# Optimization experiments

Measured on AMD Instinct MI355X. Metric: run time of the kernel, lower is better.

## Reference

```python
import jax, jax.numpy as jnp
import numpy as np

B, T, D, H, L = 128, 512, 64, 512, 256  # batch, max_seq_len, input_dim, hidden_dim, latent_dim


def setup_inputs() -> dict:
    key = jax.random.key(0)
    ks = jax.random.split(key, 12)
    x = jax.random.normal(ks[0], (B, T, D), dtype=jnp.float32)
    lengths = jax.random.randint(ks[1], (B,), 1, T + 1)
    lengths = lengths.at[0].set(T)  # ensure max(lengths) == T for static shapes
    s = 0.05
    p = lambda k, shp: jax.random.normal(k, shp, dtype=jnp.float32) * s
    return {
        "x": x, "lengths": lengths,
        # encoder LSTM (PyTorch gate order i,f,g,o); b = b_ih + b_hh fused
        "W_ih_e": p(ks[2], (4 * H, D)), "W_hh_e": p(ks[3], (4 * H, H)), "b_e": p(ks[4], (4 * H,)),
        "W_lat": p(ks[5], (L, H)), "b_lat": p(ks[6], (L,)),
        # decoder LSTM
        "W_ih_d": p(ks[7], (4 * H, L)), "W_hh_d": p(ks[8], (4 * H, H)), "b_d": p(ks[9], (4 * H,)),
        "W_out": p(ks[10], (D, H)), "b_out": p(ks[11], (D,)),
    }


def _lstm_cell(gates, c):
    # gates: [B, 4H] pre-activations in PyTorch order (input, forget, cell, output)
    i = jax.nn.sigmoid(gates[:, :H])
    f = jax.nn.sigmoid(gates[:, H:2 * H])
    g = jnp.tanh(gates[:, 2 * H:3 * H])
    o = jax.nn.sigmoid(gates[:, 3 * H:])
    c_new = f * c + i * g
    h_new = o * jnp.tanh(c_new)
    return h_new, c_new


def reference(x, lengths, W_ih_e, W_hh_e, b_e, W_lat, b_lat, W_ih_d, W_hh_d, b_d, W_out, b_out):
    mask = jnp.arange(T)[:, None] < lengths[None, :]  # [T, B] valid-step mask
    # Precompute input contributions for all timesteps: [T, B, 4H]
    gx = jnp.einsum('btd,gd->tbg', x, W_ih_e) + b_e
    h0 = jnp.zeros((B, H), x.dtype)
    c0 = jnp.zeros((B, H), x.dtype)

    # Encoder: packed semantics == freeze (h, c) once t >= length, so final h
    # equals the hidden state at each sequence's last valid step.
    def enc_step(carry, inp):
        h, c = carry
        g, m = inp
        h_new, c_new = _lstm_cell(g + h @ W_hh_e.T, c)
        m = m[:, None]
        return (jnp.where(m, h_new, h), jnp.where(m, c_new, c)), None

    (h_n, _), _ = jax.lax.scan(enc_step, (h0, c0), (gx, mask))
    z = h_n @ W_lat.T + b_lat  # [B, L]

    # Decoder input is z repeated at every valid step -> constant per-step input term.
    zx = z @ W_ih_d.T + b_d  # [B, 4H]

    def dec_step(carry, m):
        h, c = carry
        h_new, c_new = _lstm_cell(zx + h @ W_hh_d.T, c)
        m = m[:, None]
        h2 = jnp.where(m, h_new, h)
        c2 = jnp.where(m, c_new, c)
        y = jnp.where(m, h2, jnp.zeros_like(h2))  # pad_packed_sequence zero-pads outputs
        return (h2, c2), y

    _, ys = jax.lax.scan(dec_step, (h0, c0), mask)  # [T, B, H]
    # Padded positions: ys == 0, so output there is exactly b_out (matches torch).
    out = jnp.einsum('tbh,dh->btd', ys, W_out) + b_out  # [B, T, D]
    return out
```

## Files before the change

kernel.cpp:

```cpp
#include <hip/hip_runtime.h>
#include <cstdint>

constexpr int NB = 128;
constexpr int NT = 512;
constexpr int ND = 64;
constexpr int NH = 512;
constexpr int NL = 256;

typedef _Float16 half8 __attribute__((ext_vector_type(8)));
typedef float F4 __attribute__((ext_vector_type(4)));
typedef uint32_t u32;
typedef unsigned long long u64;
typedef uint32_t u32x4 __attribute__((ext_vector_type(4)));

constexpr size_t OFF_WFE = 0;
constexpr size_t OFF_WFD = (2u << 20);
constexpr size_t OFF_WFX = (4u << 20);
constexpr size_t OFF_WFO = (4u << 20) + (256u << 10);
constexpr size_t OFF_XF  = (4u << 20) + (320u << 10);
constexpr size_t OFF_RE  = (12u << 20) + (320u << 10);
constexpr size_t OFF_RD  = (13u << 20) + (320u << 10);
constexpr size_t OFF_Z   = (14u << 20) + (320u << 10);
constexpr size_t OFF_ZX  = (14u << 20) + (448u << 10);

__device__ inline float sigm(float x) {
  float e = __expf(-fabsf(x));
  float p = 1.f / (1.f + e);
  return x >= 0.f ? p : 1.f - p;
}
__device__ inline float tanh_(float x) {
  float e = __expf(-2.f * fabsf(x));
  float t = (1.f - e) / (1.f + e);
  return x >= 0.f ? t : -t;
}
__device__ inline half8 cvt8(F4 a, F4 b) {
  half8 h;
  h[0] = (_Float16)a[0]; h[1] = (_Float16)a[1]; h[2] = (_Float16)a[2]; h[3] = (_Float16)a[3];
  h[4] = (_Float16)b[0]; h[5] = (_Float16)b[1]; h[6] = (_Float16)b[2]; h[7] = (_Float16)b[3];
  return h;
}

__global__ __launch_bounds__(256) void setup_kernel(
    const float* __restrict__ x, const float* __restrict__ W_hh_e,
    const float* __restrict__ W_ih_e, const float* __restrict__ W_hh_d,
    const float* __restrict__ W_out,
    half8* __restrict__ WfE, half8* __restrict__ WfX, half8* __restrict__ WfD,
    half8* __restrict__ WfO, half8* __restrict__ Xf) {
  int c = blockIdx.x * 256 + threadIdx.x;
  if (c < 131072) {
    int hc = c >> 12, g = (c >> 10) & 3, tt = (c >> 6) & 15, l = c & 63;
    int col = g * 512 + hc * 16 + (l & 15);
    int k8 = 4 * tt + (l >> 4);
    const F4* s = (const F4*)(W_hh_e + (size_t)col * 512 + k8 * 8);
    WfE[c] = cvt8(s[0], s[1]);
  } else if (c < 147456) {
    int id = c - 131072;
    int hc = id >> 9, g = (id >> 7) & 3, tx = (id >> 6) & 1, l = id & 63;
    int col = g * 512 + hc * 16 + (l & 15);
    int k8 = 4 * tx + (l >> 4);
    const F4* s = (const F4*)(W_ih_e + (size_t)col * 64 + k8 * 8);
    WfX[id] = cvt8(s[0], s[1]);
  } else if (c < 278528) {
    int id = c - 147456;
    int hc = id >> 12, g = (id >> 10) & 3, tt = (id >> 6) & 15, l = id & 63;
    int col = g * 512 + hc * 16 + (l & 15);
    int k8 = 4 * tt + (l >> 4);
    const F4* s = (const F4*)(W_hh_d + (size_t)col * 512 + k8 * 8);
    WfD[id] = cvt8(s[0], s[1]);
  } else if (c < 282624) {
    int id = c - 278528;
    int dt = id >> 10, k = (id >> 6) & 15, l = id & 63;
    int d = dt * 16 + (l & 15);
    int k8 = k * 4 + (l >> 4);
    const F4* s = (const F4*)(W_out + (size_t)d * 512 + k8 * 8);
    WfO[id] = cvt8(s[0], s[1]);
  } else {
    int id = c - 282624;
    int t = id >> 10, bi = (id >> 7) & 7, k8 = (id >> 4) & 7, row = id & 15;
    const F4* s = (const F4*)(x + ((size_t)(bi * 16 + row) * NT + t) * ND + k8 * 8);
    Xf[id] = cvt8(s[0], s[1]);
  }
}

#define PIN4(v) asm volatile("" : "+v"(v.x), "+v"(v.y), "+v"(v.z), "+v"(v.w))

#define STAGE_H(RINGT, TAG)                                                      \
  {                                                                              \
    const u64* bp = (RINGT) + ((size_t)((TAG) & 3) * 16 + srow) * 256;           \
    u64 v[16];                                                                   \
    for (;;) {                                                                   \
      _Pragma("unroll")                                                          \
      for (int j = 0; j < 16; j++)                                               \
        v[j] = __hip_atomic_load(bp + (scb + 16 * (j >> 2)) * 4 + (j & 3),       \
                                 __ATOMIC_RELAXED, __HIP_MEMORY_SCOPE_AGENT);    \
      bool ok = true;                                                            \
      _Pragma("unroll")                                                          \
      for (int j = 0; j < 16; j++) ok &= ((u32)(v[j] >> 32) == (u32)(TAG));      \
      if (ok) break;                                                             \
      __builtin_amdgcn_s_sleep(1);                                               \
    }                                                                            \
    _Pragma("unroll")                                                            \
    for (int j = 0; j < 4; j++) {                                                \
      int cc = scb + 16 * j;                                                     \
      u32x4 u = {(u32)v[4 * j], (u32)v[4 * j + 1], (u32)v[4 * j + 2],            \
                 (u32)v[4 * j + 3]};                                             \
      Hlds[srow * 64 + (cc ^ (srow & 7))] = u;                                   \
    }                                                                            \
  }

__global__ __launch_bounds__(256, 1) void enc_persist(
    const uint4* __restrict__ Wf, const uint4* __restrict__ Wfx,
    const uint4* __restrict__ Xf, u64* __restrict__ Ring,
    const float* __restrict__ b_e, const int* __restrict__ lengths) {
  const int tid = threadIdx.x;
  const int l = tid & 63, g = tid >> 6;
  const int bi = (int)blockIdx.x & 7, w = (int)blockIdx.x >> 3;
  __shared__ u32x4 Hlds[1024];
  __shared__ float gl[4][16][17];
  __shared__ unsigned short hst[16][16];

  uint4 wb[16];
#pragma unroll
  for (int k = 0; k < 16; k++) {
    wb[k] = Wf[(size_t)w * 4096 + (g * 16 + k) * 64 + l];
    PIN4(wb[k]);
  }
  uint4 wx0 = Wfx[(size_t)w * 512 + (g * 2 + 0) * 64 + l];
  uint4 wx1 = Wfx[(size_t)w * 512 + (g * 2 + 1) * 64 + l];
  PIN4(wx0); PIN4(wx1);

  const int row = tid >> 4, col = tid & 15;
  const int b = bi * 16 + row;
  const int len = lengths[b];
  const float be0 = b_e[w * 16 + col], be1 = b_e[512 + w * 16 + col];
  const float be2 = b_e[1024 + w * 16 + col], be3 = b_e[1536 + w * 16 + col];
  float cst = 0.f, hreg = 0.f;
  const int srow = tid >> 4, scb = tid & 15;
  u64* ringT = Ring + (size_t)bi * (4 * 16 * 256);
  const int ar = l & 15, swz = ar & 7, r0 = (l >> 4) * 4;

  for (int t = 0; t < NT; t++) {
    if (t > 0) {
      STAGE_H(ringT, t);
      __syncthreads();
    }
    F4 acc0 = {0.f, 0.f, 0.f, 0.f}, acc1 = {0.f, 0.f, 0.f, 0.f};
    if (t > 0) {
#pragma unroll
      for (int k = 0; k < 16; k += 2) {
        u32x4 a0 = Hlds[ar * 64 + (((l >> 4) + 4 * k) ^ swz)];
        u32x4 a1 = Hlds[ar * 64 + (((l >> 4) + 4 * (k + 1)) ^ swz)];
        acc0 = __builtin_amdgcn_mfma_f32_16x16x32_f16(
            __builtin_bit_cast(half8, a0), __builtin_bit_cast(half8, wb[k]), acc0, 0, 0, 0);
        acc1 = __builtin_amdgcn_mfma_f32_16x16x32_f16(
            __builtin_bit_cast(half8, a1), __builtin_bit_cast(half8, wb[k + 1]), acc1, 0, 0, 0);
      }
    }
    uint4 xa0 = Xf[((size_t)t * 8 + bi) * 128 + l];
    uint4 xa1 = Xf[((size_t)t * 8 + bi) * 128 + 64 + l];
    acc0 = __builtin_amdgcn_mfma_f32_16x16x32_f16(
        __builtin_bit_cast(half8, xa0), __builtin_bit_cast(half8, wx0), acc0, 0, 0, 0);
    acc1 = __builtin_amdgcn_mfma_f32_16x16x32_f16(
        __builtin_bit_cast(half8, xa1), __builtin_bit_cast(half8, wx1), acc1, 0, 0, 0);
    F4 acc = acc0 + acc1;
#pragma unroll
    for (int r = 0; r < 4; r++) gl[g][r0 + r][ar] = acc[r];
    __syncthreads();

    float hv;
    if (t < len) {
      float gi = gl[0][row][col] + be0;
      float gf = gl[1][row][col] + be1;
      float gg = gl[2][row][col] + be2;
      float go = gl[3][row][col] + be3;
      float i = sigm(gi), f = sigm(gf), gz = tanh_(gg), o = sigm(go);
      cst = f * cst + i * gz;
      hv = o * tanh_(cst);
    } else {
      hv = hreg;
    }
    hreg = hv;
    hst[row][col] = __builtin_bit_cast(unsigned short, (_Float16)hv);
    __syncthreads();

    if (tid < 128) {
      int pr = tid >> 3, pk = tid & 7;
      u32 lo = (u32)hst[pr][2 * pk] | ((u32)hst[pr][2 * pk + 1] << 16);
      u64 vv = ((u64)(u32)(t + 1) << 32) | lo;
      __hip_atomic_store(ringT + ((size_t)((t + 1) & 3) * 16 + pr) * 256 + w * 8 + pk,
                         vv, __ATOMIC_RELAXED, __HIP_MEMORY_SCOPE_AGENT);
    }
  }
}

__global__ __launch_bounds__(256) void z_kernel(const u64* __restrict__ RingE,
                                                const float* __restrict__ W_lat,
                                                const float* __restrict__ b_lat,
                                                float* __restrict__ Z) {
  int b = blockIdx.x, lc = threadIdx.x;
  int bi = b >> 4, row = b & 15;
  const u64* hp = RingE + ((size_t)(bi * 4 + (NT & 3)) * 16 + row) * 256;
  float acc = 0.f;
  for (int j = 0; j < 256; j++) {
    u32 lo = (u32)hp[j];
    float h0 = (float)__builtin_bit_cast(_Float16, (unsigned short)(lo & 0xFFFF));
    float h1 = (float)__builtin_bit_cast(_Float16, (unsigned short)(lo >> 16));
    acc += h0 * W_lat[(size_t)lc * 512 + 2 * j] + h1 * W_lat[(size_t)lc * 512 + 2 * j + 1];
  }
  Z[(size_t)b * 256 + lc] = acc + b_lat[lc];
}

__global__ __launch_bounds__(256) void zx_kernel(const float* __restrict__ Z,
                                                 const float* __restrict__ W_ihd,
                                                 const float* __restrict__ b_d,
                                                 float* __restrict__ ZX) {
  int o = blockIdx.x * 256 + threadIdx.x;
  int b = o >> 11, gc = o & 2047;
  const F4* zp = (const F4*)(Z + (size_t)b * 256);
  const F4* wp = (const F4*)(W_ihd + (size_t)gc * 256);
  float acc = 0.f;
  for (int k4 = 0; k4 < 64; k4++) {
    F4 z = zp[k4], wv = wp[k4];
    acc += z[0] * wv[0] + z[1] * wv[1] + z[2] * wv[2] + z[3] * wv[3];
  }
  ZX[o] = acc + b_d[gc];
}

__global__ __launch_bounds__(256, 1) void dec_persist(
    const uint4* __restrict__ Wf, const uint4* __restrict__ WfO,
    u64* __restrict__ Ring, const float* __restrict__ ZX,
    const float* __restrict__ b_out, float* __restrict__ out,
    const int* __restrict__ lengths) {
  const int tid = threadIdx.x;
  const int l = tid & 63, g = tid >> 6;
  const int bi = (int)blockIdx.x & 7, w = (int)blockIdx.x >> 3;
  __shared__ u32x4 Hlds[1024];
  __shared__ float gl[4][16][17];
  __shared__ unsigned short hst[16][16];

  uint4 wb[16], wo[16];
#pragma unroll
  for (int k = 0; k < 16; k++) {
    wb[k] = Wf[(size_t)w * 4096 + (g * 16 + k) * 64 + l];
    wo[k] = WfO[(size_t)g * 1024 + k * 64 + l];
    PIN4(wb[k]); PIN4(wo[k]);
  }

  const int row = tid >> 4, col = tid & 15;
  const int b = bi * 16 + row;
  const int len = lengths[b];
  const int lenA = lengths[bi * 16 + (l & 15)];
  const float bo = b_out[g * 16 + (l & 15)];
  const float zr0 = ZX[(size_t)b * 2048 + w * 16 + col];
  const float zr1 = ZX[(size_t)b * 2048 + 512 + w * 16 + col];
  const float zr2 = ZX[(size_t)b * 2048 + 1024 + w * 16 + col];
  const float zr3 = ZX[(size_t)b * 2048 + 1536 + w * 16 + col];
  float cst = 0.f, hreg = 0.f;
  const int srow = tid >> 4, scb = tid & 15;
  u64* ringT = Ring + (size_t)bi * (4 * 16 * 256);
  const int ar = l & 15, swz = ar & 7, r0 = (l >> 4) * 4;

  for (int t = 0; t <= NT; t++) {
    if (t == NT && w != 31) break;
    if (t > 0) {
      STAGE_H(ringT, t);
      __syncthreads();
    }
    if (t < NT) {
      F4 acc0 = {0.f, 0.f, 0.f, 0.f}, acc1 = {0.f, 0.f, 0.f, 0.f};
      if (t > 0) {
#pragma unroll
        for (int k = 0; k < 16; k += 2) {
          u32x4 a0 = Hlds[ar * 64 + (((l >> 4) + 4 * k) ^ swz)];
          u32x4 a1 = Hlds[ar * 64 + (((l >> 4) + 4 * (k + 1)) ^ swz)];
          acc0 = __builtin_amdgcn_mfma_f32_16x16x32_f16(
              __builtin_bit_cast(half8, a0), __builtin_bit_cast(half8, wb[k]), acc0, 0, 0, 0);
          acc1 = __builtin_amdgcn_mfma_f32_16x16x32_f16(
              __builtin_bit_cast(half8, a1), __builtin_bit_cast(half8, wb[k + 1]), acc1, 0, 0, 0);
        }
      }
      F4 acc = acc0 + acc1;
#pragma unroll
      for (int r = 0; r < 4; r++) gl[g][r0 + r][ar] = acc[r];
      __syncthreads();

      float hv;
      if (t < len) {
        float gi = gl[0][row][col] + zr0;
        float gf = gl[1][row][col] + zr1;
        float gg = gl[2][row][col] + zr2;
        float go = gl[3][row][col] + zr3;
        float i = sigm(gi), f = sigm(gf), gz = tanh_(gg), o = sigm(go);
        cst = f * cst + i * gz;
        hv = o * tanh_(cst);
      } else {
        hv = hreg;
      }
      hreg = hv;
      hst[row][col] = __builtin_bit_cast(unsigned short, (_Float16)hv);
      __syncthreads();

      if (tid < 128) {
        int pr = tid >> 3, pk = tid & 7;
        u32 lo = (u32)hst[pr][2 * pk] | ((u32)hst[pr][2 * pk + 1] << 16);
        u64 vv = ((u64)(u32)(t + 1) << 32) | lo;
        __hip_atomic_store(ringT + ((size_t)((t + 1) & 3) * 16 + pr) * 256 + w * 8 + pk,
                           vv, __ATOMIC_RELAXED, __HIP_MEMORY_SCOPE_AGENT);
      }
    }
    if (t > 0 && w == ((t - 1) & 31)) {
      bool ma = (t - 1) < lenA;
      F4 oa0 = {0.f, 0.f, 0.f, 0.f}, oa1 = {0.f, 0.f, 0.f, 0.f};
      u32x4 zer = {0u, 0u, 0u, 0u};
#pragma unroll
      for (int k = 0; k < 16; k += 2) {
        u32x4 a0 = ma ? Hlds[ar * 64 + (((l >> 4) + 4 * k) ^ swz)] : zer;
        u32x4 a1 = ma ? Hlds[ar * 64 + (((l >> 4) + 4 * (k + 1)) ^ swz)] : zer;
        oa0 = __builtin_amdgcn_mfma_f32_16x16x32_f16(
            __builtin_bit_cast(half8, a0), __builtin_bit_cast(half8, wo[k]), oa0, 0, 0, 0);
        oa1 = __builtin_amdgcn_mfma_f32_16x16x32_f16(
            __builtin_bit_cast(half8, a1), __builtin_bit_cast(half8, wo[k + 1]), oa1, 0, 0, 0);
      }
      F4 oa = oa0 + oa1;
#pragma unroll
      for (int r = 0; r < 4; r++)
        out[((size_t)(bi * 16 + r0 + r) * NT + (t - 1)) * 64 + g * 16 + (l & 15)] = oa[r] + bo;
    }
  }
}

extern "C" void kernel_launch(void* const* d_in, const int* in_sizes, int n_in,
                              void* d_out, int out_size, void* d_ws, size_t ws_size,
                              hipStream_t stream) {
  const float* x      = (const float*)d_in[0];
  const int* lengths  = (const int*)d_in[1];
  const float* W_ih_e = (const float*)d_in[2];
  const float* W_hh_e = (const float*)d_in[3];
  const float* b_e    = (const float*)d_in[4];
  const float* W_lat  = (const float*)d_in[5];
  const float* b_lat  = (const float*)d_in[6];
  const float* W_ih_d = (const float*)d_in[7];
  const float* W_hh_d = (const float*)d_in[8];
  const float* b_d    = (const float*)d_in[9];
  const float* W_out  = (const float*)d_in[10];
  const float* b_out  = (const float*)d_in[11];
  float* out = (float*)d_out;
  char* ws = (char*)d_ws;

  half8* WfE = (half8*)(ws + OFF_WFE);
  half8* WfD = (half8*)(ws + OFF_WFD);
  half8* WfX = (half8*)(ws + OFF_WFX);
  half8* WfO = (half8*)(ws + OFF_WFO);
  half8* Xf  = (half8*)(ws + OFF_XF);
  u64* RingE = (u64*)(ws + OFF_RE);
  u64* RingD = (u64*)(ws + OFF_RD);
  float* Z  = (float*)(ws + OFF_Z);
  float* ZX = (float*)(ws + OFF_ZX);

  hipMemsetAsync(RingE, 0, 2u << 20, stream);
  setup_kernel<<<3152, 256, 0, stream>>>(x, W_hh_e, W_ih_e, W_hh_d, W_out,
                                         WfE, WfX, WfD, WfO, Xf);

  enc_persist<<<256, 256, 0, stream>>>((const uint4*)WfE, (const uint4*)WfX,
                                       (const uint4*)Xf, RingE, b_e, lengths);
  z_kernel<<<128, 256, 0, stream>>>(RingE, W_lat, b_lat, Z);
  zx_kernel<<<1024, 256, 0, stream>>>(Z, W_ih_d, b_d, ZX);
  dec_persist<<<256, 256, 0, stream>>>((const uint4*)WfD, (const uint4*)WfO,
                                       RingD, ZX, b_out, out, lengths);
}
```

Measured before the change: 3.946 ms.

## Split inter-block hidden-state exchange into separate data and per-wave tag arrays

Replaces the tagged 64-bit ring entries (data plus step tag in every word) with a packed fp16 data buffer and a small per-wave tag array. Consumers poll only 128 tags with a wave-wide vote, then read the data once. Producers pack h via lane shuffles, removing the LDS staging buffer and one block barrier per step. The x-projection load is also hoisted ahead of the wait, and the decoder's output projection is restructured. The cost is an extra release-style wait (vmcnt) before each tag store, and correctness depends on ordering between relaxed stores.

New measurement: 6.788 ms. +72.0%, slower.

```diff
diff --git a/kernel.cpp b/kernel.cpp
--- a/kernel.cpp
+++ b/kernel.cpp
@@ -18,10 +18,12 @@
 constexpr size_t OFF_WFX = (4u << 20);
 constexpr size_t OFF_WFO = (4u << 20) + (256u << 10);
 constexpr size_t OFF_XF  = (4u << 20) + (320u << 10);
-constexpr size_t OFF_RE  = (12u << 20) + (320u << 10);
-constexpr size_t OFF_RD  = (13u << 20) + (320u << 10);
-constexpr size_t OFF_Z   = (14u << 20) + (320u << 10);
-constexpr size_t OFF_ZX  = (14u << 20) + (448u << 10);
+constexpr size_t OFF_DE  = (12u << 20) + (320u << 10);
+constexpr size_t OFF_DD  = OFF_DE + (512u << 10);
+constexpr size_t OFF_TE  = OFF_DD + (512u << 10);
+constexpr size_t OFF_TD  = OFF_TE + (64u << 10);
+constexpr size_t OFF_Z   = OFF_TD + (64u << 10);
+constexpr size_t OFF_ZX  = OFF_Z + (128u << 10);
 
 __device__ inline float sigm(float x) {
   float e = __expf(-fabsf(x));
@@ -39,6 +41,10 @@
   h[4] = (_Float16)b[0]; h[5] = (_Float16)b[1]; h[6] = (_Float16)b[2]; h[7] = (_Float16)b[3];
   return h;
 }
+
+#define PIN4(v) asm volatile("" : "+v"(v.x), "+v"(v.y), "+v"(v.z), "+v"(v.w))
+#define MFMA(A, B, C) __builtin_amdgcn_mfma_f32_16x16x32_f16( \
+    __builtin_bit_cast(half8, A), __builtin_bit_cast(half8, B), C, 0, 0, 0)
 
 __global__ __launch_bounds__(256) void setup_kernel(
     const float* __restrict__ x, const float* __restrict__ W_hh_e,
@@ -82,89 +88,99 @@
   }
 }
 
-#define PIN4(v) asm volatile("" : "+v"(v.x), "+v"(v.y), "+v"(v.z), "+v"(v.w))
-
-#define STAGE_H(RINGT, TAG)                                                      \
-  {                                                                              \
-    const u64* bp = (RINGT) + ((size_t)((TAG) & 3) * 16 + srow) * 256;           \
-    u64 v[16];                                                                   \
-    for (;;) {                                                                   \
-      _Pragma("unroll")                                                          \
-      for (int j = 0; j < 16; j++)                                               \
-        v[j] = __hip_atomic_load(bp + (scb + 16 * (j >> 2)) * 4 + (j & 3),       \
-                                 __ATOMIC_RELAXED, __HIP_MEMORY_SCOPE_AGENT);    \
-      bool ok = true;                                                            \
-      _Pragma("unroll")                                                          \
-      for (int j = 0; j < 16; j++) ok &= ((u32)(v[j] >> 32) == (u32)(TAG));      \
-      if (ok) break;                                                             \
-      __builtin_amdgcn_s_sleep(1);                                               \
-    }                                                                            \
-    _Pragma("unroll")                                                            \
-    for (int j = 0; j < 4; j++) {                                                \
-      int cc = scb + 16 * j;                                                     \
-      u32x4 u = {(u32)v[4 * j], (u32)v[4 * j + 1], (u32)v[4 * j + 2],            \
-                 (u32)v[4 * j + 3]};                                             \
-      Hlds[srow * 64 + (cc ^ (srow & 7))] = u;                                   \
-    }                                                                            \
+#define POLL_TAGS(TT, T)                                                        \
+  for (;;) {                                                                    \
+    u32 ta = __hip_atomic_load((TT) + l, __ATOMIC_RELAXED,                      \
+                               __HIP_MEMORY_SCOPE_AGENT);                       \
+    u32 tb = __hip_atomic_load((TT) + 64 + l, __ATOMIC_RELAXED,                 \
+                               __HIP_MEMORY_SCOPE_AGENT);                       \
+    if (__all(ta >= (u32)(T) && tb >= (u32)(T))) break;                         \
+  }
+
+#define STAGE_DATA(DT, T)                                                       \
+  {                                                                             \
+    const u64* dp = (DT) + (size_t)((T) & 3) * 2048 + srow * 128 + scb * 8;     \
+    u64 v[8];                                                                   \
+    _Pragma("unroll")                                                           \
+    for (int j = 0; j < 8; j++)                                                 \
+      v[j] = __hip_atomic_load(dp + j, __ATOMIC_RELAXED,                        \
+                               __HIP_MEMORY_SCOPE_AGENT);                       \
+    _Pragma("unroll")                                                           \
+    for (int j = 0; j < 8; j++) {                                               \
+      int cc = scb * 4 + (j >> 1);                                              \
+      *(u64*)&lds32[srow * 256 + ((cc ^ (srow & 7)) << 2) + (j & 1) * 2] = v[j];\
+    }                                                                           \
+  }
+
+#define PUBLISH(DT, TT, HV, T)                                                  \
+  {                                                                             \
+    u32 self = (u32)__builtin_bit_cast(unsigned short, (_Float16)(HV));         \
+    u32 part = (u32)__shfl_xor((int)self, 1);                                   \
+    u32 p32 = (l & 1) ? ((self << 16) | part) : ((part << 16) | self);          \
+    u32 q = (u32)__shfl_xor((int)p32, 2);                                       \
+    u64 p64 = (l & 2) ? (((u64)p32 << 32) | q) : (((u64)q << 32) | p32);        \
+    if ((l & 3) == 0)                                                           \
+      __hip_atomic_store((DT) + (size_t)(((T) + 1) & 3) * 2048 +                \
+                             (size_t)row * 128 + w * 4 + ((l >> 2) & 3),        \
+                         p64, __ATOMIC_RELAXED, __HIP_MEMORY_SCOPE_AGENT);      \
+    asm volatile("s_waitcnt vmcnt(0)" ::: "memory");                            \
+    if (l == 0)                                                                 \
+      __hip_atomic_store((TT) + w * 4 + g, (u32)((T) + 1), __ATOMIC_RELAXED,    \
+                         __HIP_MEMORY_SCOPE_AGENT);                             \
   }
 
 __global__ __launch_bounds__(256, 1) void enc_persist(
     const uint4* __restrict__ Wf, const uint4* __restrict__ Wfx,
-    const uint4* __restrict__ Xf, u64* __restrict__ Ring,
+    const uint4* __restrict__ Xf, u64* __restrict__ Data, u32* __restrict__ Tag,
     const float* __restrict__ b_e, const int* __restrict__ lengths) {
   const int tid = threadIdx.x;
   const int l = tid & 63, g = tid >> 6;
   const int bi = (int)blockIdx.x & 7, w = (int)blockIdx.x >> 3;
-  __shared__ u32x4 Hlds[1024];
+  __shared__ u32 lds32[4096];
   __shared__ float gl[4][16][17];
-  __shared__ unsigned short hst[16][16];
 
   uint4 wb[16];
 #pragma unroll
-  for (int k = 0; k < 16; k++) {
-    wb[k] = Wf[(size_t)w * 4096 + (g * 16 + k) * 64 + l];
-    PIN4(wb[k]);
-  }
+  for (int k = 0; k < 16; k++) wb[k] = Wf[(size_t)w * 4096 + (g * 16 + k) * 64 + l];
   uint4 wx0 = Wfx[(size_t)w * 512 + (g * 2 + 0) * 64 + l];
   uint4 wx1 = Wfx[(size_t)w * 512 + (g * 2 + 1) * 64 + l];
-  PIN4(wx0); PIN4(wx1);
 
   const int row = tid >> 4, col = tid & 15;
-  const int b = bi * 16 + row;
-  const int len = lengths[b];
+  const int len = lengths[bi * 16 + row];
   const float be0 = b_e[w * 16 + col], be1 = b_e[512 + w * 16 + col];
   const float be2 = b_e[1024 + w * 16 + col], be3 = b_e[1536 + w * 16 + col];
   float cst = 0.f, hreg = 0.f;
   const int srow = tid >> 4, scb = tid & 15;
-  u64* ringT = Ring + (size_t)bi * (4 * 16 * 256);
-  const int ar = l & 15, swz = ar & 7, r0 = (l >> 4) * 4;
+  u64* DT = Data + (size_t)bi * 8192;
+  u32* TT = Tag + bi * 128;
+  const int ar = l & 15, swz = ar & 7, r0v = (l >> 4) * 4;
 
   for (int t = 0; t < NT; t++) {
-    if (t > 0) {
-      STAGE_H(ringT, t);
-      __syncthreads();
-    }
-    F4 acc0 = {0.f, 0.f, 0.f, 0.f}, acc1 = {0.f, 0.f, 0.f, 0.f};
-    if (t > 0) {
-#pragma unroll
-      for (int k = 0; k < 16; k += 2) {
-        u32x4 a0 = Hlds[ar * 64 + (((l >> 4) + 4 * k) ^ swz)];
-        u32x4 a1 = Hlds[ar * 64 + (((l >> 4) + 4 * (k + 1)) ^ swz)];
-        acc0 = __builtin_amdgcn_mfma_f32_16x16x32_f16(
-            __builtin_bit_cast(half8, a0), __builtin_bit_cast(half8, wb[k]), acc0, 0, 0, 0);
-        acc1 = __builtin_amdgcn_mfma_f32_16x16x32_f16(
-            __builtin_bit_cast(half8, a1), __builtin_bit_cast(half8, wb[k + 1]), acc1, 0, 0, 0);
-      }
-    }
+#pragma unroll
+    for (int k = 0; k < 16; k++) PIN4(wb[k]);
+    PIN4(wx0); PIN4(wx1);
     uint4 xa0 = Xf[((size_t)t * 8 + bi) * 128 + l];
     uint4 xa1 = Xf[((size_t)t * 8 + bi) * 128 + 64 + l];
-    acc0 = __builtin_amdgcn_mfma_f32_16x16x32_f16(
-        __builtin_bit_cast(half8, xa0), __builtin_bit_cast(half8, wx0), acc0, 0, 0, 0);
-    acc1 = __builtin_amdgcn_mfma_f32_16x16x32_f16(
-        __builtin_bit_cast(half8, xa1), __builtin_bit_cast(half8, wx1), acc1, 0, 0, 0);
+    if (t > 0) {
+      POLL_TAGS(TT, t);
+      STAGE_DATA(DT, t);
+      __syncthreads();
+    }
+    F4 acc0 = {0.f, 0.f, 0.f, 0.f}, acc1 = {0.f, 0.f, 0.f, 0.f};
+    acc0 = MFMA(xa0, wx0, acc0);
+    acc1 = MFMA(xa1, wx1, acc1);
+    if (t > 0) {
+#pragma unroll
+      for (int k = 0; k < 16; k += 2) {
+        u32x4 a0 = *(u32x4*)&lds32[ar * 256 + (((4 * k + (l >> 4)) ^ swz) << 2)];
+        u32x4 a1 = *(u32x4*)&lds32[ar * 256 + (((4 * (k + 1) + (l >> 4)) ^ swz) << 2)];
+        acc0 = MFMA(a0, wb[k], acc0);
+        acc1 = MFMA(a1, wb[k + 1], acc1);
+      }
+    }
     F4 acc = acc0 + acc1;
 #pragma unroll
-    for (int r = 0; r < 4; r++) gl[g][r0 + r][ar] = acc[r];
+    for (int r = 0; r < 4; r++) gl[g][r0v + r][ar] = acc[r];
     __syncthreads();
 
     float hv;
@@ -180,29 +196,20 @@
       hv = hreg;
     }
     hreg = hv;
-    hst[row][col] = __builtin_bit_cast(unsigned short, (_Float16)hv);
-    __syncthreads();
-
-    if (tid < 128) {
-      int pr = tid >> 3, pk = tid & 7;
-      u32 lo = (u32)hst[pr][2 * pk] | ((u32)hst[pr][2 * pk + 1] << 16);
-      u64 vv = ((u64)(u32)(t + 1) << 32) | lo;
-      __hip_atomic_store(ringT + ((size_t)((t + 1) & 3) * 16 + pr) * 256 + w * 8 + pk,
-                         vv, __ATOMIC_RELAXED, __HIP_MEMORY_SCOPE_AGENT);
-    }
-  }
-}
-
-__global__ __launch_bounds__(256) void z_kernel(const u64* __restrict__ RingE,
+    PUBLISH(DT, TT, hv, t);
+  }
+}
+
+__global__ __launch_bounds__(256) void z_kernel(const u32* __restrict__ DataE,
                                                 const float* __restrict__ W_lat,
                                                 const float* __restrict__ b_lat,
                                                 float* __restrict__ Z) {
   int b = blockIdx.x, lc = threadIdx.x;
   int bi = b >> 4, row = b & 15;
-  const u64* hp = RingE + ((size_t)(bi * 4 + (NT & 3)) * 16 + row) * 256;
+  const u32* hp = DataE + (size_t)bi * 16384 + (size_t)row * 256;
   float acc = 0.f;
   for (int j = 0; j < 256; j++) {
-    u32 lo = (u32)hp[j];
+    u32 lo = hp[j];
     float h0 = (float)__builtin_bit_cast(_Float16, (unsigned short)(lo & 0xFFFF));
     float h1 = (float)__builtin_bit_cast(_Float16, (unsigned short)(lo >> 16));
     acc += h0 * W_lat[(size_t)lc * 512 + 2 * j] + h1 * W_lat[(size_t)lc * 512 + 2 * j + 1];
@@ -226,24 +233,40 @@
   ZX[o] = acc + b_d[gc];
 }
 
+#define OUT_PROJ(TCUR)                                                           \
+  {                                                                              \
+    bool ma = ((TCUR) < lenA);                                                   \
+    F4 oa0 = {0.f, 0.f, 0.f, 0.f}, oa1 = {0.f, 0.f, 0.f, 0.f};                   \
+    u32x4 zer = {0u, 0u, 0u, 0u};                                                \
+    _Pragma("unroll")                                                            \
+    for (int k = 0; k < 16; k += 2) {                                            \
+      u32x4 a0 = ma ? *(u32x4*)&lds32[ar * 256 + (((4 * k + (l >> 4)) ^ swz) << 2)] : zer; \
+      u32x4 a1 = ma ? *(u32x4*)&lds32[ar * 256 + (((4 * (k + 1) + (l >> 4)) ^ swz) << 2)] : zer; \
+      oa0 = MFMA(a0, wo[k], oa0);                                                \
+      oa1 = MFMA(a1, wo[k + 1], oa1);                                            \
+    }                                                                            \
+    F4 oa = oa0 + oa1;                                                           \
+    _Pragma("unroll")                                                            \
+    for (int r = 0; r < 4; r++)                                                  \
+      out[((size_t)(bi * 16 + r0v + r) * NT + (TCUR)) * 64 + g * 16 + (l & 15)] = oa[r] + bo; \
+  }
+
 __global__ __launch_bounds__(256, 1) void dec_persist(
     const uint4* __restrict__ Wf, const uint4* __restrict__ WfO,
-    u64* __restrict__ Ring, const float* __restrict__ ZX,
+    u64* __restrict__ Data, u32* __restrict__ Tag, const float* __restrict__ ZX,
     const float* __restrict__ b_out, float* __restrict__ out,
     const int* __restrict__ lengths) {
   const int tid = threadIdx.x;
   const int l = tid & 63, g = tid >> 6;
   const int bi = (int)blockIdx.x & 7, w = (int)blockIdx.x >> 3;
-  __shared__ u32x4 Hlds[1024];
+  __shared__ u32 lds32[4096];
   __shared__ float gl[4][16][17];
-  __shared__ unsigned short hst[16][16];
 
   uint4 wb[16], wo[16];
 #pragma unroll
   for (int k = 0; k < 16; k++) {
     wb[k] = Wf[(size_t)w * 4096 + (g * 16 + k) * 64 + l];
     wo[k] = WfO[(size_t)g * 1024 + k * 64 + l];
-    PIN4(wb[k]); PIN4(wo[k]);
   }
 
   const int row = tid >> 4, col = tid & 15;
@@ -257,75 +280,57 @@
   const float zr3 = ZX[(size_t)b * 2048 + 1536 + w * 16 + col];
   float cst = 0.f, hreg = 0.f;
   const int srow = tid >> 4, scb = tid & 15;
-  u64* ringT = Ring + (size_t)bi * (4 * 16 * 256);
-  const int ar = l & 15, swz = ar & 7, r0 = (l >> 4) * 4;
-
-  for (int t = 0; t <= NT; t++) {
-    if (t == NT && w != 31) break;
+  u64* DT = Data + (size_t)bi * 8192;
+  u32* TT = Tag + bi * 128;
+  const int ar = l & 15, swz = ar & 7, r0v = (l >> 4) * 4;
+
+  for (int t = 0; t < NT; t++) {
+#pragma unroll
+    for (int k = 0; k < 16; k++) { PIN4(wb[k]); PIN4(wo[k]); }
     if (t > 0) {
-      STAGE_H(ringT, t);
+      POLL_TAGS(TT, t);
+      STAGE_DATA(DT, t);
       __syncthreads();
     }
-    if (t < NT) {
-      F4 acc0 = {0.f, 0.f, 0.f, 0.f}, acc1 = {0.f, 0.f, 0.f, 0.f};
-      if (t > 0) {
-#pragma unroll
-        for (int k = 0; k < 16; k += 2) {
-          u32x4 a0 = Hlds[ar * 64 + (((l >> 4) + 4 * k) ^ swz)];
-          u32x4 a1 = Hlds[ar * 64 + (((l >> 4) + 4 * (k + 1)) ^ swz)];
-          acc0 = __builtin_amdgcn_mfma_f32_16x16x32_f16(
-              __builtin_bit_cast(half8, a0), __builtin_bit_cast(half8, wb[k]), acc0, 0, 0, 0);
-          acc1 = __builtin_amdgcn_mfma_f32_16x16x32_f16(
-              __builtin_bit_cast(half8, a1), __builtin_bit_cast(half8, wb[k + 1]), acc1, 0, 0, 0);
-        }
+    F4 acc0 = {0.f, 0.f, 0.f, 0.f}, acc1 = {0.f, 0.f, 0.f, 0.f};
+    if (t > 0) {
+#pragma unroll
+      for (int k = 0; k < 16; k += 2) {
+        u32x4 a0 = *(u32x4*)&lds32[ar * 256 + (((4 * k + (l >> 4)) ^ swz) << 2)];
+        u32x4 a1 = *(u32x4*)&lds32[ar * 256 + (((4 * (k + 1) + (l >> 4)) ^ swz) << 2)];
+        acc0 = MFMA(a0, wb[k], acc0);
+        acc1 = MFMA(a1, wb[k + 1], acc1);
       }
-      F4 acc = acc0 + acc1;
-#pragma unroll
-      for (int r = 0; r < 4; r++) gl[g][r0 + r][ar] = acc[r];
-      __syncthreads();
-
-      float hv;
-      if (t < len) {
-        float gi = gl[0][row][col] + zr0;
-        float gf = gl[1][row][col] + zr1;
-        float gg = gl[2][row][col] + zr2;
-        float go = gl[3][row][col] + zr3;
-        float i = sigm(gi), f = sigm(gf), gz = tanh_(gg), o = sigm(go);
-        cst = f * cst + i * gz;
-        hv = o * tanh_(cst);
-      } else {
-        hv = hreg;
-      }
-      hreg = hv;
-      hst[row][col] = __builtin_bit_cast(unsigned short, (_Float16)hv);
-      __syncthreads();
-
-      if (tid < 128) {
-        int pr = tid >> 3, pk = tid & 7;
-        u32 lo = (u32)hst[pr][2 * pk] | ((u32)hst[pr][2 * pk + 1] << 16);
-        u64 vv = ((u64)(u32)(t + 1) << 32) | lo;
-        __hip_atomic_store(ringT + ((size_t)((t + 1) & 3) * 16 + pr) * 256 + w * 8 + pk,
-                           vv, __ATOMIC_RELAXED, __HIP_MEMORY_SCOPE_AGENT);
-      }
-    }
-    if (t > 0 && w == ((t - 1) & 31)) {
-      bool ma = (t - 1) < lenA;
-      F4 oa0 = {0.f, 0.f, 0.f, 0.f}, oa1 = {0.f, 0.f, 0.f, 0.f};
-      u32x4 zer = {0u, 0u, 0u, 0u};
-#pragma unroll
-      for (int k = 0; k < 16; k += 2) {
-        u32x4 a0 = ma ? Hlds[ar * 64 + (((l >> 4) + 4 * k) ^ swz)] : zer;
-        u32x4 a1 = ma ? Hlds[ar * 64 + (((l >> 4) + 4 * (k + 1)) ^ swz)] : zer;
-        oa0 = __builtin_amdgcn_mfma_f32_16x16x32_f16(
-            __builtin_bit_cast(half8, a0), __builtin_bit_cast(half8, wo[k]), oa0, 0, 0, 0);
-        oa1 = __builtin_amdgcn_mfma_f32_16x16x32_f16(
-            __builtin_bit_cast(half8, a1), __builtin_bit_cast(half8, wo[k + 1]), oa1, 0, 0, 0);
-      }
-      F4 oa = oa0 + oa1;
-#pragma unroll
-      for (int r = 0; r < 4; r++)
-        out[((size_t)(bi * 16 + r0 + r) * NT + (t - 1)) * 64 + g * 16 + (l & 15)] = oa[r] + bo;
-    }
+    }
+    F4 acc = acc0 + acc1;
+#pragma unroll
+    for (int r = 0; r < 4; r++) gl[g][r0v + r][ar] = acc[r];
+    __syncthreads();
+
+    float hv;
+    if (t < len) {
+      float gi = gl[0][row][col] + zr0;
+      float gf = gl[1][row][col] + zr1;
+      float gg = gl[2][row][col] + zr2;
+      float go = gl[3][row][col] + zr3;
+      float i = sigm(gi), f = sigm(gf), gz = tanh_(gg), o = sigm(go);
+      cst = f * cst + i * gz;
+      hv = o * tanh_(cst);
+    } else {
+      hv = hreg;
+    }
+    hreg = hv;
+    PUBLISH(DT, TT, hv, t);
+
+    if (t > 0 && w == ((t - 1) & 31)) OUT_PROJ(t - 1);
+    __syncthreads();
+  }
+
+  if (w == 31) {
+    POLL_TAGS(TT, NT);
+    STAGE_DATA(DT, NT);
+    __syncthreads();
+    OUT_PROJ(NT - 1);
   }
 }
 
@@ -352,19 +357,21 @@
   half8* WfX = (half8*)(ws + OFF_WFX);
   half8* WfO = (half8*)(ws + OFF_WFO);
   half8* Xf  = (half8*)(ws + OFF_XF);
-  u64* RingE = (u64*)(ws + OFF_RE);
-  u64* RingD = (u64*)(ws + OFF_RD);
+  u64* DataE = (u64*)(ws + OFF_DE);
+  u64* DataD = (u64*)(ws + OFF_DD);
+  u32* TagE  = (u32*)(ws + OFF_TE);
+  u32* TagD  = (u32*)(ws + OFF_TD);
   float* Z  = (float*)(ws + OFF_Z);
   float* ZX = (float*)(ws + OFF_ZX);
 
-  hipMemsetAsync(RingE, 0, 2u << 20, stream);
+  hipMemsetAsync(TagE, 0, 128u << 10, stream);
   setup_kernel<<<3152, 256, 0, stream>>>(x, W_hh_e, W_ih_e, W_hh_d, W_out,
                                          WfE, WfX, WfD, WfO, Xf);
 
   enc_persist<<<256, 256, 0, stream>>>((const uint4*)WfE, (const uint4*)WfX,
-                                       (const uint4*)Xf, RingE, b_e, lengths);
-  z_kernel<<<128, 256, 0, stream>>>(RingE, W_lat, b_lat, Z);
+                                       (const uint4*)Xf, DataE, TagE, b_e, lengths);
+  z_kernel<<<128, 256, 0, stream>>>((const u32*)DataE, W_lat, b_lat, Z);
   zx_kernel<<<1024, 256, 0, stream>>>(Z, W_ih_d, b_d, ZX);
   dec_persist<<<256, 256, 0, stream>>>((const uint4*)WfD, (const uint4*)WfO,
-                                       RingD, ZX, b_out, out, lengths);
-}
+                                       DataD, TagD, ZX, b_out, out, lengths);
+}
```
